# Kernel optimization log

Measured on AMD Instinct MI355X. Metric: run time of the kernel, lower is better.

## Reference

```python
import jax, jax.numpy as jnp
import numpy as np

H_IN, W_IN = 512, 896          # input_shape
H, W = 64, 224                 # current_shape = (h, w_expand // 6)
N_CAM = 6
NPF = 256                      # num_pos_feats
TEMP = 10000.0


def setup_inputs():
    key = jax.random.key(0)
    k0, k1, k2, k3, k4, k5 = jax.random.split(key, 6)
    b, n = 8, N_CAM
    # extrinsic: 4x4 with a near-orthonormal rotation block and translation (cam height ~1.5m)
    rot = jnp.eye(3) + 0.1 * jax.random.normal(k0, (b, n, 3, 3), dtype=jnp.float32)
    trans = jax.random.normal(k1, (b, n, 3), dtype=jnp.float32)
    trans = trans.at[..., 2].set(1.5 + 0.1 * jnp.abs(trans[..., 2]))
    extrinsic = jnp.zeros((b, n, 4, 4), dtype=jnp.float32)
    extrinsic = extrinsic.at[:, :, :3, :3].set(rot)
    extrinsic = extrinsic.at[:, :, :3, 3].set(trans)
    extrinsic = extrinsic.at[:, :, 3, 3].set(1.0)
    # intrinsic: pinhole K = [[fx,0,cx],[0,fy,cy],[0,0,1]] (well conditioned, invertible)
    fx = 800.0 + 50.0 * jax.random.normal(k2, (b, n), dtype=jnp.float32)
    fy = 800.0 + 50.0 * jax.random.normal(k3, (b, n), dtype=jnp.float32)
    cx = jnp.full((b, n), W_IN / 2.0, dtype=jnp.float32)
    cy = jnp.full((b, n), H_IN / 2.0, dtype=jnp.float32)
    intrinsic = jnp.zeros((b, n, 3, 3), dtype=jnp.float32)
    intrinsic = intrinsic.at[:, :, 0, 0].set(fx).at[:, :, 1, 1].set(fy)
    intrinsic = intrinsic.at[:, :, 0, 2].set(cx).at[:, :, 1, 2].set(cy)
    intrinsic = intrinsic.at[:, :, 2, 2].set(1.0)
    # ida (image data augmentation) matrices: scale + shift affine, invertible
    s = 0.5 + 0.05 * jax.random.uniform(k4, (b, n), dtype=jnp.float32)
    t = 10.0 * jax.random.normal(k5, (b, n, 2), dtype=jnp.float32)
    ida = jnp.zeros((b, n, 3, 3), dtype=jnp.float32)
    ida = ida.at[:, :, 0, 0].set(s).at[:, :, 1, 1].set(s)
    ida = ida.at[:, :, 0, 2].set(t[..., 0]).at[:, :, 1, 2].set(t[..., 1])
    ida = ida.at[:, :, 2, 2].set(1.0)
    return {"extrinsic": extrinsic, "intrinsic": intrinsic, "ida_mats": ida, "do_flip": 0}


def reference(extrinsic, intrinsic, ida_mats, do_flip):
    b, n = extrinsic.shape[0], extrinsic.shape[1]
    # pixel grid over the full input image, sampled at feature resolution
    x = jnp.linspace(0.0, W_IN - 1, W, dtype=jnp.float32)
    y = jnp.linspace(0.0, H_IN - 1, H, dtype=jnp.float32)
    yg, xg = jnp.meshgrid(y, x, indexing="ij")            # (H, W)
    coords = jnp.stack([xg, yg, jnp.ones_like(xg)], -1)    # (H, W, 3) homogeneous
    # combined per-camera 3x3: R @ K^{-1} @ ida^{-1}
    M = jnp.einsum("bnij,bnjk->bnik", jnp.linalg.inv(intrinsic), jnp.linalg.inv(ida_mats))
    RM = jnp.einsum("bnij,bnjk->bnik", extrinsic[:, :, :3, :3], M)
    world = jnp.einsum("bnij,hwj->bnhwi", RM, coords)      # (b, n, H, W, 3)
    # F.normalize(p=2, dim=-1): x / max(||x||, eps)
    norm = jnp.maximum(jnp.linalg.norm(world, axis=-1, keepdims=True), 1e-12)
    world = world / norm
    z = world[..., 2]
    trans_z = extrinsic[:, :, 2, 3][:, :, None, None]      # (b, n, 1, 1)
    depth = -trans_z / z
    valid = (depth > 0)[..., None]                          # (b, n, H, W, 1)
    xy = world[..., :2] * depth[..., None]                  # (b, n, H, W, 2)
    if do_flip:
        xy = xy * jnp.array([1.0, -1.0], dtype=xy.dtype)
    # cat(unbind(dim=1), dim=-2): stitch cameras along width -> (b, H, n*W, ...)
    xy = jnp.transpose(xy, (0, 2, 1, 3, 4)).reshape(b, H, n * W, 2)
    valid = jnp.transpose(valid, (0, 2, 1, 3, 4)).reshape(b, H, n * W, 1)
    # sine encoding
    half = NPF // 2
    d = jnp.arange(half, dtype=jnp.float32)
    dim_t = TEMP ** (2.0 * jnp.floor(d / 2.0) / half)       # (half,)
    p = xy[..., None] / dim_t                               # (b, H, nW, 2, half)
    px = jnp.stack([jnp.sin(p[..., 0, 0::2]), jnp.cos(p[..., 0, 1::2])], -1).reshape(b, H, n * W, half)
    py = jnp.stack([jnp.sin(p[..., 1, 0::2]), jnp.cos(p[..., 1, 1::2])], -1).reshape(b, H, n * W, half)
    pos = jnp.concatenate([py, px], axis=-1)                # (b, H, nW, NPF)
    pos = jnp.where(valid, pos, jnp.float32(0.0))
    pos = jnp.transpose(pos, (0, 3, 1, 2))                  # (b, NPF, H, nW)
    return pos, valid[..., 0]
```

## Files before the change

### kernel.cpp

```cpp
#include <hip/hip_runtime.h>
#include <math.h>

namespace {
constexpr int B    = 8;
constexpr int NCAM = 6;
constexpr int H    = 64;
constexpr int W    = 224;
constexpr int NW   = NCAM * W;
constexpr int NPF  = 256;
constexpr long long POS_ELEMS = (long long)B * NPF * H * NW;
}

__device__ __forceinline__ void inv3(const float m[9], float o[9]) {
  float a = m[0], b = m[1], c = m[2];
  float d = m[3], e = m[4], f = m[5];
  float g = m[6], h = m[7], i = m[8];
  float A  =  e * i - f * h;
  float Bm = -(d * i - f * g);
  float C  =  d * h - e * g;
  float det = a * A + b * Bm + c * C;
  float r = 1.0f / det;
  o[0] = A * r;  o[1] = -(b * i - c * h) * r; o[2] =  (b * f - c * e) * r;
  o[3] = Bm * r; o[4] =  (a * i - c * g) * r; o[5] = -(a * f - c * d) * r;
  o[6] = C * r;  o[7] = -(a * h - b * g) * r; o[8] =  (a * e - b * d) * r;
}

__device__ __forceinline__ void mm3(const float* a, const float* bm, float* o) {
#pragma unroll
  for (int i = 0; i < 3; ++i) {
#pragma unroll
    for (int j = 0; j < 3; ++j) {
      o[i * 3 + j] = fmaf(a[i * 3 + 0], bm[0 * 3 + j],
                     fmaf(a[i * 3 + 1], bm[1 * 3 + j],
                          a[i * 3 + 2] * bm[2 * 3 + j]));
    }
  }
}

__global__ __launch_bounds__(256) void ipm_pos_kernel(
    const float* __restrict__ ext, const float* __restrict__ intr,
    const float* __restrict__ ida, const int* __restrict__ do_flip,
    float* __restrict__ out, int write_valid) {
  const int tid = blockIdx.x * blockDim.x + threadIdx.x;
  const int wp = tid % NW;
  const int bh = tid / NW;
  const int h  = bh % H;
  const int b  = bh / H;
  if (b >= B) return;
  const int cam = wp / W;

  const int mi = b * NCAM + cam;
  const float* E  = ext  + mi * 16;
  const float* Km = intr + mi * 9;
  const float* Am = ida  + mi * 9;

  float R[9] = {E[0], E[1], E[2], E[4], E[5], E[6], E[8], E[9], E[10]};
  const float tz = E[11];
  float K[9], A[9];
#pragma unroll
  for (int i = 0; i < 9; ++i) { K[i] = Km[i]; A[i] = Am[i]; }

  float Ki[9], Ai[9], M[9], RM[9];
  inv3(K, Ki);
  inv3(A, Ai);
  mm3(Ki, Ai, M);
  mm3(R, M, RM);

  const int w = wp - cam * W;
  const float xp = (float)w * (895.0f / 223.0f);
  const float yp = (float)h * (511.0f / 63.0f);

  float wx = fmaf(RM[0], xp, fmaf(RM[1], yp, RM[2]));
  float wy = fmaf(RM[3], xp, fmaf(RM[4], yp, RM[5]));
  float wz = fmaf(RM[6], xp, fmaf(RM[7], yp, RM[8]));

  float norm = sqrtf(wx * wx + wy * wy + wz * wz);
  norm = fmaxf(norm, 1e-12f);
  const float nz = wz / norm;
  const float depth = -tz / nz;
  const bool valid = depth > 0.0f;
  float X = (wx / norm) * depth;
  float Y = (wy / norm) * depth;
  if (*do_flip) Y = -Y;

  const float c1 = 0.2076205059304498f;
  const size_t cs  = (size_t)H * NW;
  const size_t o00 = ((size_t)b * NPF * H + h) * NW + wp;

#pragma unroll 4
  for (int k = 0; k < 64; ++k) {
    const float t  = exp2f((float)k * c1);
    const float ay = Y / t;
    const float ax = X / t;
    float sy, cy, sx, cx;
    sincosf(ay, &sy, &cy);
    sincosf(ax, &sx, &cx);
    const size_t o = o00 + (size_t)(2 * k) * cs;
    out[o]            = valid ? sy : 0.0f;
    out[o + cs]       = valid ? cy : 0.0f;
    out[o + 128 * cs] = valid ? sx : 0.0f;
    out[o + 129 * cs] = valid ? cx : 0.0f;
  }

  if (write_valid) {
    out[POS_ELEMS + (size_t)bh * NW + wp] = valid ? 1.0f : 0.0f;
  }
}

extern "C" void kernel_launch(void* const* d_in, const int* in_sizes, int n_in,
                              void* d_out, int out_size, void* d_ws, size_t ws_size,
                              hipStream_t stream) {
  const float* ext  = (const float*)d_in[0];
  const float* intr = (const float*)d_in[1];
  const float* ida  = (const float*)d_in[2];
  const int*   flip = (const int*)d_in[3];
  float* out = (float*)d_out;

  const int total  = B * H * NW;
  const int block  = 256;
  const int grid   = (total + block - 1) / block;
  const int write_valid = ((long long)out_size > POS_ELEMS) ? 1 : 0;

  ipm_pos_kernel<<<grid, block, 0, stream>>>(ext, intr, ida, flip, out, write_valid);
}
```

Before: 705.0 us.

## Compute four pixels per thread with float4 stores and hardware sin/cos fast path

```diff
diff --git a/kernel.cpp b/kernel.cpp
--- a/kernel.cpp
+++ b/kernel.cpp
@@ -8,6 +8,7 @@
 constexpr int W    = 224;
 constexpr int NW   = NCAM * W;
 constexpr int NPF  = 256;
+constexpr int WP4  = NW / 4;
 constexpr long long POS_ELEMS = (long long)B * NPF * H * NW;
 }
 
@@ -41,13 +42,14 @@
     const float* __restrict__ ext, const float* __restrict__ intr,
     const float* __restrict__ ida, const int* __restrict__ do_flip,
     float* __restrict__ out, int write_valid) {
-  const int tid = blockIdx.x * blockDim.x + threadIdx.x;
-  const int wp = tid % NW;
-  const int bh = tid / NW;
-  const int h  = bh % H;
-  const int b  = bh / H;
+  const int t   = blockIdx.x * blockDim.x + threadIdx.x;
+  const int wp4 = t % WP4;
+  const int bh  = t / WP4;
+  const int h   = bh % H;
+  const int b   = bh / H;
   if (b >= B) return;
-  const int cam = wp / W;
+  const int wp0 = wp4 * 4;
+  const int cam = wp0 / W;
 
   const int mi = b * NCAM + cam;
   const float* E  = ext  + mi * 16;
@@ -66,44 +68,78 @@
   mm3(Ki, Ai, M);
   mm3(R, M, RM);
 
-  const int w = wp - cam * W;
-  const float xp = (float)w * (895.0f / 223.0f);
-  const float yp = (float)h * (511.0f / 63.0f);
+  const float yp   = (float)h * (511.0f / 63.0f);
+  const int   flip = *do_flip;
 
-  float wx = fmaf(RM[0], xp, fmaf(RM[1], yp, RM[2]));
-  float wy = fmaf(RM[3], xp, fmaf(RM[4], yp, RM[5]));
-  float wz = fmaf(RM[6], xp, fmaf(RM[7], yp, RM[8]));
+  float X[4], Y[4], vmask[4];
+#pragma unroll
+  for (int p = 0; p < 4; ++p) {
+    const int w = wp0 + p - cam * W;
+    const float xp = (float)w * (895.0f / 223.0f);
+    float wx = fmaf(RM[0], xp, fmaf(RM[1], yp, RM[2]));
+    float wy = fmaf(RM[3], xp, fmaf(RM[4], yp, RM[5]));
+    float wz = fmaf(RM[6], xp, fmaf(RM[7], yp, RM[8]));
+    float norm = sqrtf(wx * wx + wy * wy + wz * wz);
+    norm = fmaxf(norm, 1e-12f);
+    const float nz = wz / norm;
+    const float depth = -tz / nz;
+    const bool valid = depth > 0.0f;
+    float Xp = (wx / norm) * depth;
+    float Yp = (wy / norm) * depth;
+    if (flip) Yp = -Yp;
+    X[p] = valid ? Xp : 0.0f;
+    Y[p] = valid ? Yp : 0.0f;
+    vmask[p] = valid ? 1.0f : 0.0f;
+  }
+  const float amax = fmaxf(fmaxf(fabsf(X[0]), fabsf(X[1])),
+                           fmaxf(fabsf(X[2]), fabsf(X[3])));
+  const float amay = fmaxf(fmaxf(fabsf(Y[0]), fabsf(Y[1])),
+                           fmaxf(fabsf(Y[2]), fabsf(Y[3])));
+  const float ama  = fmaxf(amax, amay);
 
-  float norm = sqrtf(wx * wx + wy * wy + wz * wz);
-  norm = fmaxf(norm, 1e-12f);
-  const float nz = wz / norm;
-  const float depth = -tz / nz;
-  const bool valid = depth > 0.0f;
-  float X = (wx / norm) * depth;
-  float Y = (wy / norm) * depth;
-  if (*do_flip) Y = -Y;
+  const float c1     = 0.2076205059304498f;
+  const float INV2PI = 0.15915494309189535f;
+  const size_t cs  = (size_t)H * NW;
+  const size_t o00 = ((size_t)b * NPF * H + h) * NW + wp0;
 
-  const float c1 = 0.2076205059304498f;
-  const size_t cs  = (size_t)H * NW;
-  const size_t o00 = ((size_t)b * NPF * H + h) * NW + wp;
+  for (int k = 0; k < 64; ++k) {
+    const float inv_t = exp2f((float)(-k) * c1);
+    float4 vsy, vcy, vsx, vcx;
+    float sy[4], cy[4], sx[4], cx[4];
+    if (__builtin_expect(!__any(ama * inv_t > 800.0f), 1)) {
+      const float ck = inv_t * INV2PI;
+#pragma unroll
+      for (int p = 0; p < 4; ++p) {
+        const float ry = Y[p] * ck;
+        const float rx = X[p] * ck;
+        sy[p] = __builtin_amdgcn_sinf(ry);
+        cy[p] = __builtin_amdgcn_cosf(ry);
+        sx[p] = __builtin_amdgcn_sinf(rx);
+        cx[p] = __builtin_amdgcn_cosf(rx);
+      }
+    } else {
+      const float tk = exp2f((float)k * c1);
+#pragma unroll
+      for (int p = 0; p < 4; ++p) {
+        sincosf(Y[p] / tk, &sy[p], &cy[p]);
+        sincosf(X[p] / tk, &sx[p], &cx[p]);
+      }
+    }
+    vsy = make_float4(sy[0] * vmask[0], sy[1] * vmask[1], sy[2] * vmask[2], sy[3] * vmask[3]);
+    vcy = make_float4(cy[0] * vmask[0], cy[1] * vmask[1], cy[2] * vmask[2], cy[3] * vmask[3]);
+    vsx = make_float4(sx[0] * vmask[0], sx[1] * vmask[1], sx[2] * vmask[2], sx[3] * vmask[3]);
+    vcx = make_float4(cx[0] * vmask[0], cx[1] * vmask[1], cx[2] * vmask[2], cx[3] * vmask[3]);
 
-#pragma unroll 4
-  for (int k = 0; k < 64; ++k) {
-    const float t  = exp2f((float)k * c1);
-    const float ay = Y / t;
-    const float ax = X / t;
-    float sy, cy, sx, cx;
-    sincosf(ay, &sy, &cy);
-    sincosf(ax, &sx, &cx);
     const size_t o = o00 + (size_t)(2 * k) * cs;
-    out[o]            = valid ? sy : 0.0f;
-    out[o + cs]       = valid ? cy : 0.0f;
-    out[o + 128 * cs] = valid ? sx : 0.0f;
-    out[o + 129 * cs] = valid ? cx : 0.0f;
+    *(float4*)(out + o)            = vsy;
+    *(float4*)(out + o + cs)       = vcy;
+    *(float4*)(out + o + 128 * cs) = vsx;
+    *(float4*)(out + o + 129 * cs) = vcx;
   }
 
   if (write_valid) {
-    out[POS_ELEMS + (size_t)bh * NW + wp] = valid ? 1.0f : 0.0f;
+    *(float4*)(out + POS_ELEMS + (size_t)bh * NW + wp0) =
+        make_float4(vmask[0], vmask[1], vmask[2], vmask[3]);
   }
 }
 
@@ -116,9 +152,9 @@
   const int*   flip = (const int*)d_in[3];
   float* out = (float*)d_out;
 
-  const int total  = B * H * NW;
-  const int block  = 256;
-  const int grid   = (total + block - 1) / block;
+  const int total = B * H * WP4 * 4 / 4;
+  const int block = 256;
+  const int grid  = (total + block - 1) / block;
   const int write_valid = ((long long)out_size > POS_ELEMS) ? 1 : 0;
 
   ipm_pos_kernel<<<grid, block, 0, stream>>>(ext, intr, ida, flip, out, write_valid);
```

Measured after the change: 689.7 us. 2.2% less time.
